# Performance work log

Measured on AMD Instinct MI355X. Metric: run time of the kernel, lower is better.

The kernel has to match this reference:

```python
import jax, jax.numpy as jnp
import numpy as np

# --- static config (matches init_kwargs) ---
DIM = 192          # kv channels
CS = 2             # channel_scale -> q/out channels = DIM//CS
NH = 6             # num heads
WS = 4             # kv window size (q window = 2*WS)
S, H, W = 16, 32, 32          # coarse (input) resolution
SD, HD, WD = 32, 64, 64
HEAD = DIM // NH
SCALE = HEAD ** -0.5

# Relative position index: query coords are the fine-grid positions mapped to
# coarse coords via repeat_interleave(2) (as in the original coords_s/h/w),
# key coords are the coarse window positions. (Original torch code contained a
# buggy 2D->3D port of the strided key subsample; this is the consistent 3D form.)
_r = np.repeat(np.arange(WS), 2)
qc = np.stack(np.meshgrid(_r, _r, _r, indexing='ij'), -1).reshape(-1, 3)        # (512,3)
_k = np.arange(WS)
kc = np.stack(np.meshgrid(_k, _k, _k, indexing='ij'), -1).reshape(-1, 3)        # (64,3)
_rel = qc[:, None, :] - kc[None, :, :] + (WS - 1)                                # in [0, 2*WS-2]
REL_INDEX = jnp.asarray(_rel[..., 0] * (2 * WS - 1) ** 2 + _rel[..., 1] * (2 * WS - 1) + _rel[..., 2])  # (512,64)
TABLE_ROWS = (4 * WS - 1) ** 3  # as in original parameter shape


def ln(x, g, b, eps=1e-5):
    mu = jnp.mean(x, axis=-1, keepdims=True)
    var = jnp.mean(jnp.square(x - mu), axis=-1, keepdims=True)
    return (x - mu) * jax.lax.rsqrt(var + eps) * g + b


def win_part(x, ws):
    # (B,s,h,w,C) -> (B*num_windows, ws^3, C)
    B, s, h, w, C = x.shape
    x = x.reshape(B, s // ws, ws, h // ws, ws, w // ws, ws, C)
    return x.transpose(0, 1, 3, 5, 2, 4, 6, 7).reshape(-1, ws * ws * ws, C)


def win_rev(x, ws, B, s, h, w):
    # (B*num_windows, ws^3, C) -> (B,s,h,w,C)
    C = x.shape[-1]
    x = x.reshape(B, s // ws, h // ws, w // ws, ws, ws, ws, C)
    return x.transpose(0, 1, 4, 2, 5, 3, 6, 7).reshape(B, s, h, w, C)


def setup_inputs() -> dict:
    key = jax.random.key(0)
    ks = jax.random.split(key, 12)
    d = DIM
    dh = d // CS
    hid = int(dh * 4)
    f = lambda i, shape: jax.random.normal(ks[i], shape, jnp.float32) * 0.02
    return dict(
        x=jax.random.normal(ks[0], (2, S * H * W, d), jnp.float32),
        x_downsampled=jax.random.normal(ks[1], (2, SD * HD * WD, dh), jnp.float32),
        gamma1=jnp.ones((d,), jnp.float32), beta1=jnp.zeros((d,), jnp.float32),
        W_kv=f(2, (d, 2 * d)), b_kv=jnp.zeros((2 * d,), jnp.float32),
        W_q=f(3, (dh, d)), b_q=jnp.zeros((d,), jnp.float32),
        W_proj=f(4, (d, dh)), b_proj=jnp.zeros((dh,), jnp.float32),
        bias_table=f(5, (TABLE_ROWS, NH)),
        exp_gamma=jnp.ones((d,), jnp.float32), exp_beta=jnp.zeros((d,), jnp.float32),
        deconv_w=f(6, (d, dh, 2, 2, 2)), deconv_b=jnp.zeros((dh,), jnp.float32),
        gamma2=jnp.ones((dh,), jnp.float32), beta2=jnp.zeros((dh,), jnp.float32),
        W1=f(7, (dh, hid)), b1=jnp.zeros((hid,), jnp.float32),
        W2=f(8, (hid, dh)), b2=jnp.zeros((dh,), jnp.float32),
        padwh=0,
    )


def reference(x, x_downsampled, gamma1, beta1, W_kv, b_kv, W_q, b_q, W_proj, b_proj,
              bias_table, exp_gamma, exp_beta, deconv_w, deconv_b, gamma2, beta2,
              W1, b1, W2, b2, padwh):
    B = x.shape[0]
    d = DIM
    dh = d // CS
    # ---- windowed cross attention: kv from coarse x (norm1), q from fine skip ----
    kv = ln(x, gamma1, beta1).reshape(B, S, H, W, d)
    kv_w = win_part(kv, WS)                                           # (Bw, 64, d)
    q_w = win_part(x_downsampled.reshape(B, SD, HD, WD, dh), 2 * WS)  # (Bw, 512, dh)
    Bw, N, _ = kv_w.shape
    Nq = q_w.shape[1]
    kvp = kv_w @ W_kv + b_kv                                          # (Bw, N, 2d)
    k, v = jnp.split(kvp, 2, axis=-1)
    k = k.reshape(Bw, N, NH, HEAD).transpose(0, 2, 1, 3)
    v = v.reshape(Bw, N, NH, HEAD).transpose(0, 2, 1, 3)
    q = (q_w @ W_q + b_q).reshape(Bw, Nq, NH, HEAD).transpose(0, 2, 1, 3) * SCALE
    attn = jnp.einsum('bhqd,bhkd->bhqk', q, k)                        # (Bw, NH, 512, 64)
    bias = bias_table[REL_INDEX].transpose(2, 0, 1)                   # (NH, 512, 64)
    attn = jax.nn.softmax(attn + bias[None], axis=-1)
    out = jnp.einsum('bhqk,bhkd->bhqd', attn, v).transpose(0, 2, 1, 3).reshape(Bw, Nq, d)
    out = out @ W_proj + b_proj                                       # (Bw, Nq, dh)
    out = win_rev(out, 2 * WS, B, SD, HD, WD).reshape(B, SD * HD * WD, dh)
    # ---- Patch_Expanding residual: LN + ConvTranspose3d(k=2, s=2) ----
    xe = ln(x, exp_gamma, exp_beta).reshape(B, S, H, W, d)
    sc = jnp.einsum('bshwc,coijk->bsihjwko', xe, deconv_w) + deconv_b  # (B,S,2,H,2,W,2,dh)
    sc = sc.reshape(B, SD * HD * WD, dh)
    # ---- residual + MLP ----
    y = sc + out
    hdn = jax.nn.gelu(ln(y, gamma2, beta2) @ W1 + b1, approximate=False)
    return y + (hdn @ W2 + b2)
```

## Files before the change

### kernel.cpp

```cpp
#include <hip/hip_runtime.h>
#include <math.h>

#define ATT_SCALE 0.17677669529663687f

typedef __bf16 bf16x8 __attribute__((ext_vector_type(8)));
typedef __bf16 bf16x4 __attribute__((ext_vector_type(4)));
typedef float  f32x4  __attribute__((ext_vector_type(4)));

#define MFMA16(a,b,c) __builtin_amdgcn_mfma_f32_16x16x32_bf16(a,b,c,0,0,0)

#define BIAS_BYTES 786432
#define WKV_OFF 0
#define WQ_OFF  73728
#define WP_OFF  92160
#define WD_OFF  110592
#define W1_OFF  258048
#define W2_OFF  294912
#define NSWZ    331776

static __device__ __forceinline__ float gelu_exact(float v){
    return 0.5f * v * (1.0f + erff(v * 0.70710678118654752f));
}

static __device__ __forceinline__ bf16x8 afrag(const __bf16* w, int NRT, int kt, int rt, int lane){
    return ((const bf16x8*)w)[(kt*NRT + rt)*64 + lane];
}

__global__ __launch_bounds__(256) void k_prep(const float* __restrict__ table,
    const float* __restrict__ Wkv, const float* __restrict__ Wq,
    const float* __restrict__ Wp,  const float* __restrict__ Wd,
    const float* __restrict__ W1,  const float* __restrict__ W2,
    float* __restrict__ bias, __bf16* __restrict__ wsw){
    int id = blockIdx.x * 256 + threadIdx.x;
    if (id < 196608){
        int k  = id & 63;
        int qg = (id >> 6) & 511;
        int h  = id >> 15;
        int qi = qg >> 6, qj = (qg >> 3) & 7, qk = qg & 7;
        int ki = k >> 4,  kj = (k >> 2) & 3,  kk = k & 3;
        int r0 = (qi >> 1) - ki + 3;
        int r1 = (qj >> 1) - kj + 3;
        int r2 = (qk >> 1) - kk + 3;
        bias[id] = table[((r0 * 7 + r1) * 7 + r2) * 6 + h];
        return;
    }
    id -= 196608;
    if (id >= NSWZ) return;
    if (id >= WD_OFF && id < W1_OFF){
        int lid  = id - WD_OFF;
        int j    = lid & 7, lane = (lid >> 3) & 63, tile = lid >> 9;
        int rt   = tile % 24;
        int kt2  = tile / 24;
        int ii   = kt2 / 6, kt = kt2 % 6;
        int n    = rt * 16 + (lane & 15);
        int o    = n % 96, jk = n / 96;
        int kdim = kt * 32 + (lane >> 4) * 8 + j;
        wsw[id] = (__bf16)(Wd[(kdim * 96 + o) * 8 + ii * 4 + jk]);
        return;
    }
    const float* W; int N, NRT, off; float sc = 1.f;
    if      (id < WQ_OFF){ W = Wkv; N = 384; NRT = 24; off = WKV_OFF; }
    else if (id < WP_OFF){ W = Wq;  N = 192; NRT = 12; off = WQ_OFF; sc = ATT_SCALE; }
    else if (id < WD_OFF){ W = Wp;  N = 96;  NRT = 6;  off = WP_OFF; }
    else if (id < W2_OFF){ W = W1;  N = 384; NRT = 24; off = W1_OFF; }
    else                 { W = W2;  N = 96;  NRT = 6;  off = W2_OFF; }
    int lid  = id - off;
    int j    = lid & 7, lane = (lid >> 3) & 63, tile = lid >> 9;
    int rt   = tile % NRT, kt = tile / NRT;
    int n    = rt * 16 + (lane & 15);
    int k    = kt * 32 + (lane >> 4) * 8 + j;
    wsw[id + 0] = (__bf16)(W[k * N + n] * sc);
}

__global__ __launch_bounds__(512) void k_attn(const float* __restrict__ x,
    const float* __restrict__ xd, const float* __restrict__ g1, const float* __restrict__ b1v,
    const float* __restrict__ bkv, const float* __restrict__ bq, const float* __restrict__ bpj,
    const __bf16* __restrict__ wsw, const float* __restrict__ bias, float* __restrict__ yout){
    __shared__ __bf16 Qs[64][196];
    __shared__ __bf16 Ks[64][196];
    __shared__ __bf16 Vt[192][68];
    __shared__ __bf16 Wqp_s[36864];
    const int tid = threadIdx.x, lane = tid & 63, w = tid >> 6;
    const int win = blockIdx.x, b = win >> 8, wrem = win & 255;
    const int sw_ = wrem >> 6, hw_ = (wrem >> 3) & 7, ww_ = wrem & 7;

    #pragma unroll
    for (int i = 0; i < 9; i++)
        ((uint4*)Wqp_s)[tid + 512*i] = ((const uint4*)(wsw + WQ_OFF))[tid + 512*i];

    {
        int row = tid >> 3, sub = tid & 7;
        int si = row >> 4, hi = (row >> 2) & 3, wi = row & 3;
        int ci = ((b * 16 + 4 * sw_ + si) * 32 + 4 * hw_ + hi) * 32 + 4 * ww_ + wi;
        const float* xp = x + ci * 192 + sub * 24;
        float v[24]; float s = 0.f, ss = 0.f;
        #pragma unroll
        for (int i = 0; i < 6; i++){
            float4 t = ((const float4*)xp)[i];
            v[4*i] = t.x; v[4*i+1] = t.y; v[4*i+2] = t.z; v[4*i+3] = t.w;
            s += t.x + t.y + t.z + t.w;
            ss += t.x*t.x + t.y*t.y + t.z*t.z + t.w*t.w;
        }
        #pragma unroll
        for (int m = 1; m < 8; m <<= 1){ s += __shfl_xor(s, m); ss += __shfl_xor(ss, m); }
        float mu = s * (1.f/192.f), var = ss * (1.f/192.f) - mu*mu, rs = rsqrtf(var + 1e-5f);
        #pragma unroll
        for (int i = 0; i < 3; i++){
            bf16x8 t;
            #pragma unroll
            for (int jj = 0; jj < 8; jj++){
                int c = sub*24 + 8*i + jj;
                t[jj] = (__bf16)((v[8*i+jj] - mu) * rs * g1[c] + b1v[c]);
            }
            *(bf16x8*)&Qs[row][sub*24 + 8*i] = t;
        }
    }
    __syncthreads();
    {
        const int ct = w & 3, rh = w >> 2;
        const int tok = ct * 16 + (lane & 15);
        bf16x8 bfr[6];
        #pragma unroll
        for (int kt = 0; kt < 6; kt++) bfr[kt] = *(const bf16x8*)&Qs[tok][kt*32 + (lane>>4)*8];
        #pragma unroll
        for (int i = 0; i < 12; i++){
            int rt = rh * 12 + i;
            f32x4 acc = {0.f,0.f,0.f,0.f};
            #pragma unroll
            for (int kt = 0; kt < 6; kt++) acc = MFMA16(afrag(wsw + WKV_OFF, 24, kt, rt, lane), bfr[kt], acc);
            int cb = rt * 16 + ((lane >> 4) << 2);
            float4 b4 = *(const float4*)&bkv[cb];
            acc[0] += b4.x; acc[1] += b4.y; acc[2] += b4.z; acc[3] += b4.w;
            if (cb < 192){
                bf16x4 t;
                #pragma unroll
                for (int r = 0; r < 4; r++) t[r] = (__bf16)acc[r];
                *(bf16x4*)&Ks[tok][cb] = t;
            } else {
                #pragma unroll
                for (int r = 0; r < 4; r++) Vt[cb - 192 + r][tok] = (__bf16)acc[r];
            }
        }
    }
    __syncthreads();

    const int li_ = lane & 15, gt_ = lane >> 4, rsel = lane >> 5;

    for (int qt = 0; qt < 8; qt++){
        {
            const int ct = w & 3, rh = w >> 2;
            const int ql = ct * 16 + (lane & 15);
            const int ft = ((b * 32 + 8 * sw_ + qt) * 64 + 8 * hw_ + (ql >> 3)) * 64 + 8 * ww_ + (ql & 7);
            bf16x8 bfr[3];
            #pragma unroll
            for (int kt = 0; kt < 3; kt++){
                const float* xp = xd + ft * 96 + kt * 32 + (lane >> 4) * 8;
                float4 t0 = *(const float4*)xp;
                float4 t1 = *(const float4*)(xp + 4);
                bf16x8 t;
                t[0]=(__bf16)t0.x; t[1]=(__bf16)t0.y; t[2]=(__bf16)t0.z; t[3]=(__bf16)t0.w;
                t[4]=(__bf16)t1.x; t[5]=(__bf16)t1.y; t[6]=(__bf16)t1.z; t[7]=(__bf16)t1.w;
                bfr[kt] = t;
            }
            #pragma unroll
            for (int i = 0; i < 6; i++){
                int rt = rh * 6 + i;
                f32x4 acc = {0.f,0.f,0.f,0.f};
                #pragma unroll
                for (int kt = 0; kt < 3; kt++) acc = MFMA16(afrag(Wqp_s, 12, kt, rt, lane), bfr[kt], acc);
                int cb = rt * 16 + ((lane >> 4) << 2);
                float4 b4 = *(const float4*)&bq[cb];
                bf16x4 t;
                t[0] = (__bf16)(acc[0] + b4.x * ATT_SCALE);
                t[1] = (__bf16)(acc[1] + b4.y * ATT_SCALE);
                t[2] = (__bf16)(acc[2] + b4.z * ATT_SCALE);
                t[3] = (__bf16)(acc[3] + b4.w * ATT_SCALE);
                *(bf16x4*)&Qs[ql][cb] = t;
            }
        }
        __syncthreads();
        f32x4 ov[3][2];
        #pragma unroll
        for (int ui = 0; ui < 3; ui++){
            const int u = w * 3 + ui;
            const int h = u >> 2, qct = u & 3;
            f32x4 sc[4];
            __builtin_amdgcn_s_setprio(1);
            #pragma unroll
            for (int rt = 0; rt < 4; rt++){
                bf16x8 a  = *(const bf16x8*)&Ks[rt*16 + li_][h*32 + gt_*8];
                bf16x8 bq8 = *(const bf16x8*)&Qs[qct*16 + li_][h*32 + gt_*8];
                f32x4 z = {0.f,0.f,0.f,0.f};
                sc[rt] = MFMA16(a, bq8, z);
            }
            __builtin_amdgcn_s_setprio(0);
            const int qg = qt * 64 + qct * 16 + li_;
            const float* bp = bias + (h * 512 + qg) * 64 + (gt_ << 2);
            #pragma unroll
            for (int rt = 0; rt < 4; rt++){
                float4 b4 = *(const float4*)(bp + rt * 16);
                sc[rt][0] += b4.x; sc[rt][1] += b4.y; sc[rt][2] += b4.z; sc[rt][3] += b4.w;
            }
            float m = sc[0][0];
            #pragma unroll
            for (int rt = 0; rt < 4; rt++)
                #pragma unroll
                for (int r = 0; r < 4; r++) m = fmaxf(m, sc[rt][r]);
            m = fmaxf(m, __shfl_xor(m, 16));
            m = fmaxf(m, __shfl_xor(m, 32));
            float sum = 0.f;
            #pragma unroll
            for (int rt = 0; rt < 4; rt++)
                #pragma unroll
                for (int r = 0; r < 4; r++){ float e = __expf(sc[rt][r] - m); sc[rt][r] = e; sum += e; }
            sum += __shfl_xor(sum, 16);
            sum += __shfl_xor(sum, 32);
            float inv = 1.f / sum;
            unsigned pwv[4][2];
            #pragma unroll
            for (int rt = 0; rt < 4; rt++){
                union { __bf16 hh[2]; unsigned u; } c0, c1;
                c0.hh[0] = (__bf16)(sc[rt][0] * inv); c0.hh[1] = (__bf16)(sc[rt][1] * inv);
                c1.hh[0] = (__bf16)(sc[rt][2] * inv); c1.hh[1] = (__bf16)(sc[rt][3] * inv);
                pwv[rt][0] = c0.u; pwv[rt][1] = c1.u;
            }
            unsigned bfw[2][4];
            #pragma unroll
            for (int kt = 0; kt < 2; kt++){
                #pragma unroll
                for (int t = 0; t < 4; t++){
                    int gs   = ((gt_ & 1) << 1) + (t >> 1);
                    int addr = (((gs << 4) + li_) << 2);
                    int w0 = __builtin_amdgcn_ds_bpermute(addr, (int)pwv[2*kt + 0][t & 1]);
                    int w1 = __builtin_amdgcn_ds_bpermute(addr, (int)pwv[2*kt + 1][t & 1]);
                    bfw[kt][t] = rsel ? (unsigned)w1 : (unsigned)w0;
                }
            }
            union { unsigned u[4]; bf16x8 v; } pb0, pb1;
            #pragma unroll
            for (int t = 0; t < 4; t++){ pb0.u[t] = bfw[0][t]; pb1.u[t] = bfw[1][t]; }
            __builtin_amdgcn_s_setprio(1);
            #pragma unroll
            for (int dt = 0; dt < 2; dt++){
                f32x4 o = {0.f,0.f,0.f,0.f};
                bf16x8 a0 = *(const bf16x8*)&Vt[h*32 + dt*16 + li_][gt_*8];
                bf16x8 a1 = *(const bf16x8*)&Vt[h*32 + dt*16 + li_][32 + gt_*8];
                o = MFMA16(a0, pb0.v, o);
                o = MFMA16(a1, pb1.v, o);
                ov[ui][dt] = o;
            }
            __builtin_amdgcn_s_setprio(0);
        }
        __syncthreads();
        #pragma unroll
        for (int ui = 0; ui < 3; ui++){
            const int u = w * 3 + ui;
            const int h = u >> 2, qct = u & 3;
            const int tok = qct * 16 + li_;
            #pragma unroll
            for (int dt = 0; dt < 2; dt++){
                int cb = h * 32 + dt * 16 + (gt_ << 2);
                bf16x4 t;
                #pragma unroll
                for (int r = 0; r < 4; r++) t[r] = (__bf16)ov[ui][dt][r];
                *(bf16x4*)&Qs[tok][cb] = t;
            }
        }
        __syncthreads();
        {
            const int ct = w & 3, rh = w >> 2;
            const int ql = ct * 16 + (lane & 15);
            const int ft = ((b * 32 + 8 * sw_ + qt) * 64 + 8 * hw_ + (ql >> 3)) * 64 + 8 * ww_ + (ql & 7);
            bf16x8 bfr[6];
            #pragma unroll
            for (int kt = 0; kt < 6; kt++) bfr[kt] = *(const bf16x8*)&Qs[ql][kt*32 + (lane>>4)*8];
            #pragma unroll
            for (int i = 0; i < 3; i++){
                int rt = rh * 3 + i;
                f32x4 acc = {0.f,0.f,0.f,0.f};
                #pragma unroll
                for (int kt = 0; kt < 6; kt++) acc = MFMA16(afrag(Wqp_s + 18432, 6, kt, rt, lane), bfr[kt], acc);
                int cb = rt * 16 + ((lane >> 4) << 2);
                float4 b4 = *(const float4*)&bpj[cb];
                float4 res;
                res.x = acc[0] + b4.x;
                res.y = acc[1] + b4.y;
                res.z = acc[2] + b4.z;
                res.w = acc[3] + b4.w;
                *(float4*)&yout[ft * 96 + cb] = res;
            }
        }
        __syncthreads();
    }
}

__global__ __launch_bounds__(512) void k_mlp(const float* __restrict__ x,
    const float* __restrict__ eg, const float* __restrict__ eb,
    const float* __restrict__ g2, const float* __restrict__ b2v,
    const __bf16* __restrict__ wsw, const float* __restrict__ db,
    const float* __restrict__ b1m, const float* __restrict__ b2m,
    float* __restrict__ outp){
    __shared__ __bf16 xe[32][200];
    __shared__ float  ysl[64][100];
    __shared__ __bf16 yln[64][104];
    __shared__ __bf16 hsm[64][200];
    const int tid = threadIdx.x, lane = tid & 63, w = tid >> 6;
    const int t0 = blockIdx.x * 64;
    const int bb   = t0 >> 17;
    const int sbar = (t0 >> 12) & 31;
    const int hbar = (t0 >> 6) & 63;
    const int iD = sbar & 1, jD = hbar & 1;
    const int sc_ = sbar >> 1, hc_ = hbar >> 1;

    float4 apf[3];
    {
        int rowP = tid >> 3, subP = tid & 7;
        const float* ap = outp + (t0 + rowP) * 96 + subP * 12;
        apf[0] = ((const float4*)ap)[0];
        apf[1] = ((const float4*)ap)[1];
        apf[2] = ((const float4*)ap)[2];
    }

    {
        int row = tid >> 4, sub = tid & 15;
        int ci = ((bb * 16 + sc_) * 32 + hc_) * 32 + row;
        const float* xp = x + ci * 192 + sub * 12;
        float v[12]; float s = 0.f, ss = 0.f;
        #pragma unroll
        for (int i2 = 0; i2 < 3; i2++){
            float4 t = ((const float4*)xp)[i2];
            v[4*i2] = t.x; v[4*i2+1] = t.y; v[4*i2+2] = t.z; v[4*i2+3] = t.w;
            s += t.x + t.y + t.z + t.w;
            ss += t.x*t.x + t.y*t.y + t.z*t.z + t.w*t.w;
        }
        #pragma unroll
        for (int m = 1; m < 16; m <<= 1){ s += __shfl_xor(s, m); ss += __shfl_xor(ss, m); }
        float mu = s * (1.f/192.f), var = ss * (1.f/192.f) - mu*mu, rs = rsqrtf(var + 1e-5f);
        #pragma unroll
        for (int i2 = 0; i2 < 3; i2++){
            bf16x4 t;
            #pragma unroll
            for (int jj = 0; jj < 4; jj++){
                int c = sub*12 + 4*i2 + jj;
                t[jj] = (__bf16)((v[4*i2+jj] - mu) * rs * eg[c] + eb[c]);
            }
            *(bf16x4*)&xe[row][sub*12 + 4*i2] = t;
        }
    }
    __syncthreads();
    {
        const int li = lane & 15, gt = lane >> 4;
        const int ctD = w & 1, rhD = w >> 1;
        const int wcol = ctD * 16 + li;
        bf16x8 bfrD[6];
        #pragma unroll
        for (int kt = 0; kt < 6; kt++) bfrD[kt] = *(const bf16x8*)&xe[wcol][kt*32 + gt*8];
        const __bf16* wd = wsw + WD_OFF + iD * 73728;
        #pragma unroll
        for (int i2 = 0; i2 < 3; i2++){
            int rtl = rhD * 3 + i2;
            int rt  = 12 * jD + rtl;
            f32x4 acc = {0.f,0.f,0.f,0.f};
            #pragma unroll
            for (int kt = 0; kt < 6; kt++) acc = MFMA16(afrag(wd, 24, kt, rt, lane), bfrD[kt], acc);
            int mp   = rtl * 16 + (gt << 2);
            int kpar = (mp >= 96) ? 1 : 0;
            int o    = mp - 96 * kpar;
            int tok  = 2 * wcol + kpar;
            float4 d4 = *(const float4*)&db[o];
            float4 res;
            res.x = acc[0] + d4.x; res.y = acc[1] + d4.y;
            res.z = acc[2] + d4.z; res.w = acc[3] + d4.w;
            *(float4*)&ysl[tok][o] = res;
        }
    }
    __syncthreads();
    {
        int row = tid >> 3, sub = tid & 7;
        float v[12]; float s = 0.f, ss = 0.f;
        #pragma unroll
        for (int i2 = 0; i2 < 3; i2++){
            float4 t = apf[i2];
            float4 s4 = *(const float4*)&ysl[row][sub*12 + 4*i2];
            t.x += s4.x; t.y += s4.y; t.z += s4.z; t.w += s4.w;
            v[4*i2] = t.x; v[4*i2+1] = t.y; v[4*i2+2] = t.z; v[4*i2+3] = t.w;
            s += t.x + t.y + t.z + t.w;
            ss += t.x*t.x + t.y*t.y + t.z*t.z + t.w*t.w;
            *(float4*)&ysl[row][sub*12 + 4*i2] = t;
        }
        #pragma unroll
        for (int m = 1; m < 8; m <<= 1){ s += __shfl_xor(s, m); ss += __shfl_xor(ss, m); }
        float mu = s * (1.f/96.f), var = ss * (1.f/96.f) - mu*mu, rs = rsqrtf(var + 1e-5f);
        #pragma unroll
        for (int i2 = 0; i2 < 3; i2++){
            bf16x4 t;
            #pragma unroll
            for (int jj = 0; jj < 4; jj++){
                int c = sub*12 + 4*i2 + jj;
                t[jj] = (__bf16)((v[4*i2+jj] - mu) * rs * g2[c] + b2v[c]);
            }
            *(bf16x4*)&yln[row][sub*12 + 4*i2] = t;
        }
    }
    __syncthreads();
    const int ct = w & 3, rh = w >> 2;
    const int tok = ct * 16 + (lane & 15);
    bf16x8 bfrY[3];
    #pragma unroll
    for (int kt = 0; kt < 3; kt++) bfrY[kt] = *(const bf16x8*)&yln[tok][kt*32 + (lane>>4)*8];
    f32x4 oacc[3];
    #pragma unroll
    for (int i = 0; i < 3; i++){ f32x4 z = {0.f,0.f,0.f,0.f}; oacc[i] = z; }

    #pragma unroll
    for (int hh = 0; hh < 2; hh++){
        #pragma unroll
        for (int i = 0; i < 6; i++){
            int rtl = rh * 6 + i;
            int rtg = hh * 12 + rtl;
            f32x4 acc = {0.f,0.f,0.f,0.f};
            #pragma unroll
            for (int kt = 0; kt < 3; kt++) acc = MFMA16(afrag(wsw + W1_OFF, 24, kt, rtg, lane), bfrY[kt], acc);
            int cb = rtl * 16 + ((lane >> 4) << 2);
            float4 b4 = *(const float4*)&b1m[hh * 192 + cb];
            bf16x4 t;
            t[0] = (__bf16)gelu_exact(acc[0] + b4.x);
            t[1] = (__bf16)gelu_exact(acc[1] + b4.y);
            t[2] = (__bf16)gelu_exact(acc[2] + b4.z);
            t[3] = (__bf16)gelu_exact(acc[3] + b4.w);
            *(bf16x4*)&hsm[tok][cb] = t;
        }
        __syncthreads();
        bf16x8 bfrH[6];
        #pragma unroll
        for (int kt = 0; kt < 6; kt++) bfrH[kt] = *(const bf16x8*)&hsm[tok][kt*32 + (lane>>4)*8];
        #pragma unroll
        for (int i = 0; i < 3; i++){
            int rt = rh * 3 + i;
            #pragma unroll
            for (int kt = 0; kt < 6; kt++)
                oacc[i] = MFMA16(afrag(wsw + W2_OFF, 6, hh * 6 + kt, rt, lane), bfrH[kt], oacc[i]);
        }
        __syncthreads();
    }
    #pragma unroll
    for (int i = 0; i < 3; i++){
        int rt = rh * 3 + i;
        int cb = rt * 16 + ((lane >> 4) << 2);
        float4 b4 = *(const float4*)&b2m[cb];
        float4 yv = *(const float4*)&ysl[tok][cb];
        float4 res;
        res.x = yv.x + oacc[i][0] + b4.x;
        res.y = yv.y + oacc[i][1] + b4.y;
        res.z = yv.z + oacc[i][2] + b4.z;
        res.w = yv.w + oacc[i][3] + b4.w;
        *(float4*)&outp[(t0 + tok) * 96 + cb] = res;
    }
}

extern "C" void kernel_launch(void* const* d_in, const int* in_sizes, int n_in,
                              void* d_out, int out_size, void* d_ws, size_t ws_size,
                              hipStream_t stream){
    const float* x    = (const float*)d_in[0];
    const float* xd   = (const float*)d_in[1];
    const float* g1   = (const float*)d_in[2];
    const float* b1v  = (const float*)d_in[3];
    const float* Wkv  = (const float*)d_in[4];
    const float* bkv  = (const float*)d_in[5];
    const float* Wq   = (const float*)d_in[6];
    const float* bq   = (const float*)d_in[7];
    const float* Wp   = (const float*)d_in[8];
    const float* bpj  = (const float*)d_in[9];
    const float* btab = (const float*)d_in[10];
    const float* eg   = (const float*)d_in[11];
    const float* eb   = (const float*)d_in[12];
    const float* dw   = (const float*)d_in[13];
    const float* db   = (const float*)d_in[14];
    const float* g2   = (const float*)d_in[15];
    const float* b2v  = (const float*)d_in[16];
    const float* W1   = (const float*)d_in[17];
    const float* b1m  = (const float*)d_in[18];
    const float* W2   = (const float*)d_in[19];
    const float* b2m  = (const float*)d_in[20];
    (void)in_sizes; (void)n_in; (void)out_size; (void)ws_size;

    float*   out  = (float*)d_out;
    float*   bias = (float*)d_ws;
    __bf16*  wsw  = (__bf16*)((char*)d_ws + BIAS_BYTES);

    k_prep<<<2064, 256, 0, stream>>>(btab, Wkv, Wq, Wp, dw, W1, W2, bias, wsw);
    k_attn<<<512, 512, 0, stream>>>(x, xd, g1, b1v, bkv, bq, bpj, wsw, bias, out);
    k_mlp <<<4096, 512, 0, stream>>>(x, eg, eb, g2, b2v, wsw, db, b1m, b2m, out);
}
```

Before: 303.0 us.

## Prefetch MFMA weight fragments into registers ahead of use in MLP kernel

Weight A-fragments for the deconvolution, W1 and W2 GEMMs in the MLP kernel are loaded from global memory into registers earlier, before the barriers and LayerNorm phases that precede their use. This lets the global-load latency overlap with other work instead of stalling each MFMA chain. The two-pass hidden loop is manually unrolled and W2 fragments are double-staged in halves. The cost is much higher register pressure (dozens of bf16x8 fragments live at once), which can reduce occupancy or cause spills at 512 threads per block.

```diff
diff --git a/kernel.cpp b/kernel.cpp
--- a/kernel.cpp
+++ b/kernel.cpp
@@ -311,6 +311,8 @@
     const int hbar = (t0 >> 6) & 63;
     const int iD = sbar & 1, jD = hbar & 1;
     const int sc_ = sbar >> 1, hc_ = hbar >> 1;
+    const int ct = w & 3, rh = w >> 2;
+    const int tok = ct * 16 + (lane & 15);
 
     float4 apf[3];
     {
@@ -320,6 +322,16 @@
         apf[1] = ((const float4*)ap)[1];
         apf[2] = ((const float4*)ap)[2];
     }
+    bf16x8 afD[3][6];
+    {
+        const int rhD = w >> 1;
+        const __bf16* wd = wsw + WD_OFF + iD * 73728;
+        #pragma unroll
+        for (int i2 = 0; i2 < 3; i2++)
+            #pragma unroll
+            for (int kt = 0; kt < 6; kt++)
+                afD[i2][kt] = afrag(wd, 24, kt, 12 * jD + rhD * 3 + i2, lane);
+    }
 
     {
         int row = tid >> 4, sub = tid & 15;
@@ -348,6 +360,7 @@
         }
     }
     __syncthreads();
+    bf16x8 af1a[6][3];
     {
         const int li = lane & 15, gt = lane >> 4;
         const int ctD = w & 1, rhD = w >> 1;
@@ -355,24 +368,27 @@
         bf16x8 bfrD[6];
         #pragma unroll
         for (int kt = 0; kt < 6; kt++) bfrD[kt] = *(const bf16x8*)&xe[wcol][kt*32 + gt*8];
-        const __bf16* wd = wsw + WD_OFF + iD * 73728;
         #pragma unroll
         for (int i2 = 0; i2 < 3; i2++){
             int rtl = rhD * 3 + i2;
-            int rt  = 12 * jD + rtl;
             f32x4 acc = {0.f,0.f,0.f,0.f};
             #pragma unroll
-            for (int kt = 0; kt < 6; kt++) acc = MFMA16(afrag(wd, 24, kt, rt, lane), bfrD[kt], acc);
+            for (int kt = 0; kt < 6; kt++) acc = MFMA16(afD[i2][kt], bfrD[kt], acc);
             int mp   = rtl * 16 + (gt << 2);
             int kpar = (mp >= 96) ? 1 : 0;
             int o    = mp - 96 * kpar;
-            int tok  = 2 * wcol + kpar;
+            int tokD = 2 * wcol + kpar;
             float4 d4 = *(const float4*)&db[o];
             float4 res;
             res.x = acc[0] + d4.x; res.y = acc[1] + d4.y;
             res.z = acc[2] + d4.z; res.w = acc[3] + d4.w;
-            *(float4*)&ysl[tok][o] = res;
-        }
+            *(float4*)&ysl[tokD][o] = res;
+        }
+        #pragma unroll
+        for (int i = 0; i < 6; i++)
+            #pragma unroll
+            for (int kt = 0; kt < 3; kt++)
+                af1a[i][kt] = afrag(wsw + W1_OFF, 24, kt, rh * 6 + i, lane);
     }
     __syncthreads();
     {
@@ -403,8 +419,6 @@
         }
     }
     __syncthreads();
-    const int ct = w & 3, rh = w >> 2;
-    const int tok = ct * 16 + (lane & 15);
     bf16x8 bfrY[3];
     #pragma unroll
     for (int kt = 0; kt < 3; kt++) bfrY[kt] = *(const bf16x8*)&yln[tok][kt*32 + (lane>>4)*8];
@@ -412,41 +426,92 @@
     #pragma unroll
     for (int i = 0; i < 3; i++){ f32x4 z = {0.f,0.f,0.f,0.f}; oacc[i] = z; }
 
-    #pragma unroll
-    for (int hh = 0; hh < 2; hh++){
-        #pragma unroll
-        for (int i = 0; i < 6; i++){
-            int rtl = rh * 6 + i;
-            int rtg = hh * 12 + rtl;
-            f32x4 acc = {0.f,0.f,0.f,0.f};
-            #pragma unroll
-            for (int kt = 0; kt < 3; kt++) acc = MFMA16(afrag(wsw + W1_OFF, 24, kt, rtg, lane), bfrY[kt], acc);
-            int cb = rtl * 16 + ((lane >> 4) << 2);
-            float4 b4 = *(const float4*)&b1m[hh * 192 + cb];
-            bf16x4 t;
-            t[0] = (__bf16)gelu_exact(acc[0] + b4.x);
-            t[1] = (__bf16)gelu_exact(acc[1] + b4.y);
-            t[2] = (__bf16)gelu_exact(acc[2] + b4.z);
-            t[3] = (__bf16)gelu_exact(acc[3] + b4.w);
-            *(bf16x4*)&hsm[tok][cb] = t;
-        }
-        __syncthreads();
+    bf16x8 af2[3][3];
+    #pragma unroll
+    for (int i = 0; i < 6; i++){
+        f32x4 acc = {0.f,0.f,0.f,0.f};
+        #pragma unroll
+        for (int kt = 0; kt < 3; kt++) acc = MFMA16(af1a[i][kt], bfrY[kt], acc);
+        int cb = (rh * 6 + i) * 16 + ((lane >> 4) << 2);
+        float4 b4 = *(const float4*)&b1m[cb];
+        bf16x4 t;
+        t[0] = (__bf16)gelu_exact(acc[0] + b4.x);
+        t[1] = (__bf16)gelu_exact(acc[1] + b4.y);
+        t[2] = (__bf16)gelu_exact(acc[2] + b4.z);
+        t[3] = (__bf16)gelu_exact(acc[3] + b4.w);
+        *(bf16x4*)&hsm[tok][cb] = t;
+    }
+    #pragma unroll
+    for (int i = 0; i < 3; i++)
+        #pragma unroll
+        for (int kt = 0; kt < 3; kt++)
+            af2[i][kt] = afrag(wsw + W2_OFF, 6, kt, rh * 3 + i, lane);
+    __syncthreads();
+    {
         bf16x8 bfrH[6];
         #pragma unroll
         for (int kt = 0; kt < 6; kt++) bfrH[kt] = *(const bf16x8*)&hsm[tok][kt*32 + (lane>>4)*8];
         #pragma unroll
-        for (int i = 0; i < 3; i++){
-            int rt = rh * 3 + i;
-            #pragma unroll
-            for (int kt = 0; kt < 6; kt++)
-                oacc[i] = MFMA16(afrag(wsw + W2_OFF, 6, hh * 6 + kt, rt, lane), bfrH[kt], oacc[i]);
-        }
-        __syncthreads();
+        for (int i = 0; i < 3; i++)
+            #pragma unroll
+            for (int kt = 0; kt < 3; kt++) oacc[i] = MFMA16(af2[i][kt], bfrH[kt], oacc[i]);
+        #pragma unroll
+        for (int i = 0; i < 3; i++)
+            #pragma unroll
+            for (int kt = 0; kt < 3; kt++)
+                af2[i][kt] = afrag(wsw + W2_OFF, 6, 3 + kt, rh * 3 + i, lane);
+        #pragma unroll
+        for (int i = 0; i < 3; i++)
+            #pragma unroll
+            for (int kt = 0; kt < 3; kt++) oacc[i] = MFMA16(af2[i][kt], bfrH[3 + kt], oacc[i]);
+    }
+    #pragma unroll
+    for (int i = 0; i < 6; i++)
+        #pragma unroll
+        for (int kt = 0; kt < 3; kt++)
+            af1a[i][kt] = afrag(wsw + W1_OFF, 24, kt, 12 + rh * 6 + i, lane);
+    __syncthreads();
+    #pragma unroll
+    for (int i = 0; i < 6; i++){
+        f32x4 acc = {0.f,0.f,0.f,0.f};
+        #pragma unroll
+        for (int kt = 0; kt < 3; kt++) acc = MFMA16(af1a[i][kt], bfrY[kt], acc);
+        int cb = (rh * 6 + i) * 16 + ((lane >> 4) << 2);
+        float4 b4 = *(const float4*)&b1m[192 + cb];
+        bf16x4 t;
+        t[0] = (__bf16)gelu_exact(acc[0] + b4.x);
+        t[1] = (__bf16)gelu_exact(acc[1] + b4.y);
+        t[2] = (__bf16)gelu_exact(acc[2] + b4.z);
+        t[3] = (__bf16)gelu_exact(acc[3] + b4.w);
+        *(bf16x4*)&hsm[tok][cb] = t;
+    }
+    #pragma unroll
+    for (int i = 0; i < 3; i++)
+        #pragma unroll
+        for (int kt = 0; kt < 3; kt++)
+            af2[i][kt] = afrag(wsw + W2_OFF, 6, 6 + kt, rh * 3 + i, lane);
+    __syncthreads();
+    {
+        bf16x8 bfrH[6];
+        #pragma unroll
+        for (int kt = 0; kt < 6; kt++) bfrH[kt] = *(const bf16x8*)&hsm[tok][kt*32 + (lane>>4)*8];
+        #pragma unroll
+        for (int i = 0; i < 3; i++)
+            #pragma unroll
+            for (int kt = 0; kt < 3; kt++) oacc[i] = MFMA16(af2[i][kt], bfrH[kt], oacc[i]);
+        #pragma unroll
+        for (int i = 0; i < 3; i++)
+            #pragma unroll
+            for (int kt = 0; kt < 3; kt++)
+                af2[i][kt] = afrag(wsw + W2_OFF, 6, 9 + kt, rh * 3 + i, lane);
+        #pragma unroll
+        for (int i = 0; i < 3; i++)
+            #pragma unroll
+            for (int kt = 0; kt < 3; kt++) oacc[i] = MFMA16(af2[i][kt], bfrH[3 + kt], oacc[i]);
     }
     #pragma unroll
     for (int i = 0; i < 3; i++){
-        int rt = rh * 3 + i;
-        int cb = rt * 16 + ((lane >> 4) << 2);
+        int cb = (rh * 3 + i) * 16 + ((lane >> 4) << 2);
         float4 b4 = *(const float4*)&b2m[cb];
         float4 yv = *(const float4*)&ysl[tok][cb];
         float4 res;
```

Result: slower. 329.8 us (+8.8%).
